# Kernel tuning notes

Hardware: AMD Instinct MI355X
Metric: run time of the kernel (lower is better)

The kernel has to match this reference:

```python
import jax, jax.numpy as jnp
import numpy as np

K_SIZE = 7   # kernel_size
DIL = 2      # dilation
PAD = 6      # padding; satisfies 2*PAD == DIL*(K_SIZE-1) so unfold L == H*W


def _unfold(x, k, d, p):
    # Mimics F.pad(mode='replicate') + nn.Unfold(kernel, dilation=d, stride=1)
    # followed by view(B, C, k*k, H, W). Channel-major, kernel rows then cols.
    B, C, H, W = x.shape
    xp = jnp.pad(x, ((0, 0), (0, 0), (p, p), (p, p)), mode='edge')
    cols = jnp.stack(
        [xp[:, :, i * d:i * d + H, j * d:j * d + W]
         for i in range(k) for j in range(k)], axis=2)
    return cols  # [B, C, k*k, H, W]


def setup_inputs() -> dict:
    key = jax.random.key(0)
    ks = jax.random.split(key, 5)
    B, Cin, Cout, H, W = 2, 64, 64, 128, 128
    x = jax.random.normal(ks[0], (B, Cin, H, W), jnp.float32)
    s_in = 1.0 / np.sqrt(Cin)
    s_out = 1.0 / np.sqrt(Cout)
    Wk = jax.random.uniform(ks[1], (Cout, Cin), jnp.float32, -s_in, s_in)
    Wq = jax.random.uniform(ks[2], (Cout, Cin), jnp.float32, -s_in, s_in)
    Wv = jax.random.uniform(ks[3], (Cout, Cin), jnp.float32, -s_in, s_in)
    Wt = jax.random.uniform(ks[4], (Cin, Cout), jnp.float32, -s_out, s_out)
    return {"x": x, "Wk": Wk, "Wq": Wq, "Wv": Wv, "Wt": Wt}


def reference(x, Wk, Wq, Wv, Wt):
    # 1x1 convs (bias=False) as channel contractions + ReLU
    K = jax.nn.relu(jnp.einsum('oi,bihw->bohw', Wk, x))
    Q = jax.nn.relu(jnp.einsum('oi,bihw->bohw', Wq, x))
    V = jax.nn.relu(jnp.einsum('oi,bihw->bohw', Wv, x))
    Ku = _unfold(K, K_SIZE, DIL, PAD)   # [B, C, k2, H, W]
    Vu = _unfold(V, K_SIZE, DIL, PAD)   # [B, C, k2, H, W]
    # scores over the k2 dilated neighbors of each pixel (q dim == 1)
    A = jnp.einsum('bckhw,bchw->bkhw', Ku, Q)
    A = jax.nn.softmax(A, axis=1)       # softmax over k2 (torch dim=1)
    out = jnp.einsum('bckhw,bkhw->bchw', Vu, A)
    return jnp.einsum('oi,bihw->bohw', Wt, out) + x
```

## Files before the change

### kernel.cpp

```cpp
#include <hip/hip_runtime.h>
#include <hip/hip_bf16.h>

#define HH 128
#define WW 128
#define HWSZ (HH * WW)
#define CC 64
#define BB 2
#define KK 7
#define K2 49
#define ROWE 280

typedef unsigned int u32;

__device__ __forceinline__ int clampi(int v, int lo, int hi) {
    return v < lo ? lo : (v > hi ? hi : v);
}

__device__ __forceinline__ uint4 ld16(const __hip_bfloat16* src) {
    uint4 d; __builtin_memcpy(&d, src, 16); return d;
}

__device__ __forceinline__ void unpack8(uint4 d, float* f) {
    f[0] = __uint_as_float(d.x << 16); f[1] = __uint_as_float(d.x & 0xffff0000u);
    f[2] = __uint_as_float(d.y << 16); f[3] = __uint_as_float(d.y & 0xffff0000u);
    f[4] = __uint_as_float(d.z << 16); f[5] = __uint_as_float(d.z & 0xffff0000u);
    f[6] = __uint_as_float(d.w << 16); f[7] = __uint_as_float(d.w & 0xffff0000u);
}

__device__ __forceinline__ unsigned short f2bf(float v) {
    __hip_bfloat16 b = __float2bfloat16(v);
    return *reinterpret_cast<unsigned short*>(&b);
}

__device__ __forceinline__ int lane_off(int w) {
    const int parity = w & 1, t = w >> 1, phase = t & 1;
    return parity * 140 + phase * 70 + (t - phase);
}

__global__ __launch_bounds__(256) void kqv_kernel(
    const float* __restrict__ x,  const float* __restrict__ Wk,
    const float* __restrict__ Wq, const float* __restrict__ Wv,
    __hip_bfloat16* __restrict__ Kp, __hip_bfloat16* __restrict__ Qt,
    __hip_bfloat16* __restrict__ Vp)
{
    __shared__ __align__(16) float Wl[64][32];
    __shared__ __hip_bfloat16 T[32][2][128];

    const int xcd   = blockIdx.x & 7;
    const int t     = blockIdx.x >> 3;
    const int pbl   = t & 15;
    const int slice = t >> 4;
    const int pb    = xcd * 16 + pbl;
    const int a     = slice >> 1;
    const int ohb   = (slice & 1) * 32;
    const int b0    = pb >> 6;
    const int h0    = 2 * (pb & 63);
    const int hw0   = (pb & 63) * 256;

    const float* Wsel = (a == 0) ? Wk : (a == 1) ? Wq : Wv;

    for (int idx = threadIdx.x; idx < 2048; idx += 256) {
        const int c  = idx >> 5;
        const int ol = idx & 31;
        Wl[c][ol] = Wsel[(ohb + ol) * CC + c];
    }
    __syncthreads();

    const int quad = threadIdx.x & 63;
    const int oct  = threadIdx.x >> 6;

    const float* xbase = x + (size_t)b0 * CC * HWSZ + hw0 + quad * 4;

    float acc[8][4];
#pragma unroll
    for (int i = 0; i < 8; ++i)
#pragma unroll
        for (int j = 0; j < 4; ++j) acc[i][j] = 0.f;

#pragma unroll 4
    for (int c = 0; c < CC; ++c) {
        const float4 x4 = *(const float4*)(xbase + (size_t)c * HWSZ);
        const float xj[4] = {x4.x, x4.y, x4.z, x4.w};
        float w8[8];
        *(float4*)(w8)     = *(const float4*)&Wl[c][oct * 8];
        *(float4*)(w8 + 4) = *(const float4*)&Wl[c][oct * 8 + 4];
#pragma unroll
        for (int i = 0; i < 8; ++i)
#pragma unroll
            for (int j = 0; j < 4; ++j)
                acc[i][j] = fmaf(w8[i], xj[j], acc[i][j]);
    }

#pragma unroll
    for (int i = 0; i < 8; ++i) {
        const int ol = oct * 8 + i;
#pragma unroll
        for (int j = 0; j < 4; ++j) {
            const int px = quad * 4 + j;
            T[ol][px >> 7][px & 127] = __float2bfloat16(fmaxf(acc[i][j], 0.f));
        }
    }
    __syncthreads();

    if (a == 1) {
        for (int idx = threadIdx.x; idx < 1024; idx += 256) {
            const int px = idx >> 2;
            const int ck = idx & 3;
            unsigned short e[8];
#pragma unroll
            for (int u = 0; u < 8; ++u) {
                __hip_bfloat16 bv = T[ck * 8 + u][px >> 7][px & 127];
                e[u] = *reinterpret_cast<unsigned short*>(&bv);
            }
            __hip_bfloat16* dst = Qt +
                (size_t)(b0 * HWSZ + hw0 + px) * CC + ohb + ck * 8;
            __builtin_memcpy(dst, e, 16);
        }
    } else {
        __hip_bfloat16* arrp = (a == 0) ? Kp : Vp;
        for (int idx = threadIdx.x; idx < 2240; idx += 256) {
            const int row_id = idx / 35;
            const int cki    = idx - row_id * 35;
            const int ol     = row_id >> 1;
            const int rr     = row_id & 1;
            unsigned short e[8];
#pragma unroll
            for (int u = 0; u < 8; ++u) {
                const int q      = cki * 8 + u;
                const int parity = q >= 140 ? 1 : 0;
                const int sslot  = q - parity * 140;
                const int phase  = sslot >= 70 ? 1 : 0;
                const int local  = sslot - phase * 70;
                const int pix    = clampi(2 * (local - (phase ? 2 : 3)) + parity,
                                          0, 127);
                __hip_bfloat16 bv = T[ol][rr][pix];
                e[u] = *reinterpret_cast<unsigned short*>(&bv);
            }
            __hip_bfloat16* dst = arrp +
                ((size_t)(b0 * CC + ohb + ol) * HH + (h0 + rr)) * ROWE + cki * 8;
            __builtin_memcpy(dst, e, 16);
        }
    }
}

__global__ __launch_bounds__(256) void attn_kernel(
    const __hip_bfloat16* __restrict__ Kp, const __hip_bfloat16* __restrict__ Qt,
    const __hip_bfloat16* __restrict__ Vp, const float* __restrict__ Wt,
    const float* __restrict__ x, float* __restrict__ out)
{
    __shared__ float part[2][K2][33];
    __shared__ __align__(16) float Wt_l[64][65];
    __shared__ __align__(16) __hip_bfloat16 O_l[32][72];

    const int xcd  = blockIdx.x & 7;
    const int s    = blockIdx.x >> 3;
    const int bh   = xcd * 32 + (s >> 2);
    const int wseg = s & 3;
    const int b    = bh >> 7;
    const int h    = bh & 127;

    const int tid = threadIdx.x;
    const int px  = (tid & 15) | ((tid >> 7) << 4);
    const int cq  = (tid >> 4) & 7;
    const int w   = wseg * 32 + px;
    const int p   = b * HWSZ + h * WW + w;
    const int c0  = cq * 8;

    for (int idx = tid; idx < 4096; idx += 256)
        Wt_l[idx >> 6][idx & 63] = Wt[idx];

    int hn[KK];
#pragma unroll
    for (int i = 0; i < KK; ++i) hn[i] = clampi(h + 2 * i - 6, 0, HH - 1);

    const int loff = lane_off(w);
    const size_t cstride = (size_t)HH * ROWE;
    const __hip_bfloat16* Kc = Kp + (size_t)(b * CC + c0) * cstride + loff;
    const __hip_bfloat16* Vc = Vp + (size_t)(b * CC + c0) * cstride + loff;

    float qf[8];
    unpack8(ld16(Qt + (size_t)p * CC + c0), qf);

    float sc[K2];
#pragma unroll
    for (int k = 0; k < K2; ++k) sc[k] = 0.f;

    for (int ci = 0; ci < 8; ++ci) {
        uint4 kd[KK];
        const __hip_bfloat16* base = Kc + (size_t)ci * cstride;
#pragma unroll
        for (int i = 0; i < KK; ++i) kd[i] = ld16(base + (size_t)hn[i] * ROWE);
        const float qv = qf[ci];
#pragma unroll
        for (int i = 0; i < KK; ++i) {
            float kf[8];
            unpack8(kd[i], kf);
#pragma unroll
            for (int j = 0; j < KK; ++j)
                sc[i * KK + j] = fmaf(kf[j], qv, sc[i * KK + j]);
        }
    }

#pragma unroll
    for (int k = 0; k < K2; ++k) sc[k] += __shfl_xor(sc[k], 16, 64);
#pragma unroll
    for (int k = 0; k < K2; ++k) sc[k] += __shfl_xor(sc[k], 32, 64);

    const int sl = (tid >> 6) & 1;
    if (((tid >> 4) & 3) == 0) {
#pragma unroll
        for (int k = 0; k < K2; ++k) part[sl][k][px] = sc[k];
    }
    __syncthreads();

#pragma unroll
    for (int k = 0; k < K2; ++k) sc[k] = part[0][k][px] + part[1][k][px];
    float m = sc[0];
#pragma unroll
    for (int k = 1; k < K2; ++k) m = fmaxf(m, sc[k]);
    float sum = 0.f;
#pragma unroll
    for (int k = 0; k < K2; ++k) { sc[k] = __expf(sc[k] - m); sum += sc[k]; }
    const float inv = 1.f / sum;
#pragma unroll
    for (int k = 0; k < K2; ++k) sc[k] *= inv;

    const int hw = h * WW + w;
    float fin[8];
#pragma unroll
    for (int i = 0; i < 8; ++i)
        fin[i] = x[((size_t)(b * CC) + c0 + i) * HWSZ + hw];

    unsigned short ob[8];
    for (int ci = 0; ci < 8; ++ci) {
        uint4 vd[KK];
        const __hip_bfloat16* base = Vc + (size_t)ci * cstride;
#pragma unroll
        for (int i = 0; i < KK; ++i) vd[i] = ld16(base + (size_t)hn[i] * ROWE);
        float acc = 0.f;
#pragma unroll
        for (int i = 0; i < KK; ++i) {
            float vf[8];
            unpack8(vd[i], vf);
#pragma unroll
            for (int j = 0; j < KK; ++j)
                acc = fmaf(vf[j], sc[i * KK + j], acc);
        }
        ob[ci] = f2bf(acc);
    }

    u32 od[4];
#pragma unroll
    for (int i = 0; i < 4; ++i)
        od[i] = (u32)ob[2 * i] | ((u32)ob[2 * i + 1] << 16);
    __builtin_memcpy(&O_l[px][c0], od, 16);
    __syncthreads();

#pragma unroll
    for (int c8 = 0; c8 < 8; ++c8) {
        uint4 d = *(const uint4*)&O_l[px][c8 * 8];
        float oc[8];
        unpack8(d, oc);
#pragma unroll
        for (int cc = 0; cc < 8; ++cc) {
            const int c = c8 * 8 + cc;
#pragma unroll
            for (int i = 0; i < 8; ++i)
                fin[i] = fmaf(Wt_l[c0 + i][c], oc[cc], fin[i]);
        }
    }

#pragma unroll
    for (int i = 0; i < 8; ++i)
        out[((size_t)(b * CC) + c0 + i) * HWSZ + hw] = fin[i];
}

extern "C" void kernel_launch(void* const* d_in, const int* in_sizes, int n_in,
                              void* d_out, int out_size, void* d_ws, size_t ws_size,
                              hipStream_t stream)
{
    const float* x  = (const float*)d_in[0];
    const float* Wk = (const float*)d_in[1];
    const float* Wq = (const float*)d_in[2];
    const float* Wv = (const float*)d_in[3];
    const float* Wt = (const float*)d_in[4];
    float* out = (float*)d_out;

    const size_t KP_ELEMS = (size_t)BB * CC * HH * ROWE;
    __hip_bfloat16* Kp = (__hip_bfloat16*)d_ws;
    __hip_bfloat16* Vp = Kp + KP_ELEMS;
    __hip_bfloat16* Qt = Vp + KP_ELEMS;

    hipLaunchKernelGGL(kqv_kernel, dim3(768), dim3(256), 0, stream,
                       x, Wk, Wq, Wv, Kp, Qt, Vp);
    hipLaunchKernelGGL(attn_kernel, dim3(1024), dim3(256), 0, stream,
                       Kp, Qt, Vp, Wt, x, out);
}
```

Baseline: 65.58 us.

## Fuse K/Q/V projections into one block per image row to reuse x loads

```diff
diff --git a/kernel.cpp b/kernel.cpp
--- a/kernel.cpp
+++ b/kernel.cpp
@@ -37,108 +37,107 @@
     return parity * 140 + phase * 70 + (t - phase);
 }
 
-__global__ __launch_bounds__(256) void kqv_kernel(
+__global__ __launch_bounds__(1024) void kqv_kernel(
     const float* __restrict__ x,  const float* __restrict__ Wk,
     const float* __restrict__ Wq, const float* __restrict__ Wv,
     __hip_bfloat16* __restrict__ Kp, __hip_bfloat16* __restrict__ Qt,
     __hip_bfloat16* __restrict__ Vp)
 {
-    __shared__ __align__(16) float Wl[64][32];
-    __shared__ __hip_bfloat16 T[32][2][128];
-
-    const int xcd   = blockIdx.x & 7;
-    const int t     = blockIdx.x >> 3;
-    const int pbl   = t & 15;
-    const int slice = t >> 4;
-    const int pb    = xcd * 16 + pbl;
-    const int a     = slice >> 1;
-    const int ohb   = (slice & 1) * 32;
-    const int b0    = pb >> 6;
-    const int h0    = 2 * (pb & 63);
-    const int hw0   = (pb & 63) * 256;
-
-    const float* Wsel = (a == 0) ? Wk : (a == 1) ? Wq : Wv;
-
-    for (int idx = threadIdx.x; idx < 2048; idx += 256) {
-        const int c  = idx >> 5;
-        const int ol = idx & 31;
-        Wl[c][ol] = Wsel[(ohb + ol) * CC + c];
+    __shared__ __align__(16) float Wl[64][192];
+    __shared__ __hip_bfloat16 T[64][128];
+
+    const int xcd = blockIdx.x & 7;
+    const int s   = blockIdx.x >> 3;
+    const int rid = xcd * 32 + s;
+    const int b   = rid >> 7;
+    const int h   = rid & 127;
+
+    const int tid  = threadIdx.x;
+    const int duo  = tid & 63;
+    const int oset = tid >> 6;
+    const int oc0  = oset * 4;
+
+    for (int idx = tid; idx < 64 * 192; idx += 1024) {
+        const int c   = idx / 192;
+        const int col = idx - c * 192;
+        const int a   = col >> 6;
+        const int och = col & 63;
+        const float* Wa = (a == 0) ? Wk : (a == 1) ? Wq : Wv;
+        Wl[c][col] = Wa[och * CC + c];
     }
     __syncthreads();
 
-    const int quad = threadIdx.x & 63;
-    const int oct  = threadIdx.x >> 6;
-
-    const float* xbase = x + (size_t)b0 * CC * HWSZ + hw0 + quad * 4;
-
-    float acc[8][4];
-#pragma unroll
-    for (int i = 0; i < 8; ++i)
-#pragma unroll
-        for (int j = 0; j < 4; ++j) acc[i][j] = 0.f;
+    const float* xrow = x + (size_t)b * CC * HWSZ + h * WW + duo * 2;
+
+    float acc[3][4][2];
+#pragma unroll
+    for (int a = 0; a < 3; ++a)
+#pragma unroll
+        for (int i = 0; i < 4; ++i)
+#pragma unroll
+            for (int j = 0; j < 2; ++j) acc[a][i][j] = 0.f;
 
 #pragma unroll 4
     for (int c = 0; c < CC; ++c) {
-        const float4 x4 = *(const float4*)(xbase + (size_t)c * HWSZ);
-        const float xj[4] = {x4.x, x4.y, x4.z, x4.w};
-        float w8[8];
-        *(float4*)(w8)     = *(const float4*)&Wl[c][oct * 8];
-        *(float4*)(w8 + 4) = *(const float4*)&Wl[c][oct * 8 + 4];
-#pragma unroll
-        for (int i = 0; i < 8; ++i)
-#pragma unroll
-            for (int j = 0; j < 4; ++j)
-                acc[i][j] = fmaf(w8[i], xj[j], acc[i][j]);
-    }
-
-#pragma unroll
-    for (int i = 0; i < 8; ++i) {
-        const int ol = oct * 8 + i;
-#pragma unroll
-        for (int j = 0; j < 4; ++j) {
-            const int px = quad * 4 + j;
-            T[ol][px >> 7][px & 127] = __float2bfloat16(fmaxf(acc[i][j], 0.f));
-        }
-    }
-    __syncthreads();
-
-    if (a == 1) {
-        for (int idx = threadIdx.x; idx < 1024; idx += 256) {
-            const int px = idx >> 2;
-            const int ck = idx & 3;
+        const float2 x2 = *(const float2*)(xrow + (size_t)c * HWSZ);
+        const float xj[2] = {x2.x, x2.y};
+#pragma unroll
+        for (int a = 0; a < 3; ++a) {
+            const float4 w4 = *(const float4*)&Wl[c][a * 64 + oc0];
+            const float wi[4] = {w4.x, w4.y, w4.z, w4.w};
+#pragma unroll
+            for (int i = 0; i < 4; ++i)
+#pragma unroll
+                for (int j = 0; j < 2; ++j)
+                    acc[a][i][j] = fmaf(wi[i], xj[j], acc[a][i][j]);
+        }
+    }
+
+#pragma unroll
+    for (int a = 0; a < 3; ++a) {
+        __syncthreads();
+#pragma unroll
+        for (int i = 0; i < 4; ++i)
+#pragma unroll
+            for (int j = 0; j < 2; ++j)
+                T[oc0 + i][duo * 2 + j] =
+                    __float2bfloat16(fmaxf(acc[a][i][j], 0.f));
+        __syncthreads();
+
+        if (a == 1) {
+            const int px = tid >> 3;
+            const int ck = tid & 7;
             unsigned short e[8];
 #pragma unroll
             for (int u = 0; u < 8; ++u) {
-                __hip_bfloat16 bv = T[ck * 8 + u][px >> 7][px & 127];
+                __hip_bfloat16 bv = T[ck * 8 + u][px];
                 e[u] = *reinterpret_cast<unsigned short*>(&bv);
             }
             __hip_bfloat16* dst = Qt +
-                (size_t)(b0 * HWSZ + hw0 + px) * CC + ohb + ck * 8;
+                (size_t)(b * HWSZ + h * WW + px) * CC + ck * 8;
             __builtin_memcpy(dst, e, 16);
-        }
-    } else {
-        __hip_bfloat16* arrp = (a == 0) ? Kp : Vp;
-        for (int idx = threadIdx.x; idx < 2240; idx += 256) {
-            const int row_id = idx / 35;
-            const int cki    = idx - row_id * 35;
-            const int ol     = row_id >> 1;
-            const int rr     = row_id & 1;
-            unsigned short e[8];
-#pragma unroll
-            for (int u = 0; u < 8; ++u) {
-                const int q      = cki * 8 + u;
-                const int parity = q >= 140 ? 1 : 0;
-                const int sslot  = q - parity * 140;
-                const int phase  = sslot >= 70 ? 1 : 0;
-                const int local  = sslot - phase * 70;
-                const int pix    = clampi(2 * (local - (phase ? 2 : 3)) + parity,
-                                          0, 127);
-                __hip_bfloat16 bv = T[ol][rr][pix];
-                e[u] = *reinterpret_cast<unsigned short*>(&bv);
+        } else {
+            __hip_bfloat16* arrp = (a == 0) ? Kp : Vp;
+            for (int idx = tid; idx < 64 * 35; idx += 1024) {
+                const int och = idx / 35;
+                const int cki = idx - och * 35;
+                unsigned short e[8];
+#pragma unroll
+                for (int u = 0; u < 8; ++u) {
+                    const int q      = cki * 8 + u;
+                    const int parity = q >= 140 ? 1 : 0;
+                    const int sslot  = q - parity * 140;
+                    const int phase  = sslot >= 70 ? 1 : 0;
+                    const int local  = sslot - phase * 70;
+                    const int pix    = clampi(
+                        2 * (local - (phase ? 2 : 3)) + parity, 0, 127);
+                    __hip_bfloat16 bv = T[och][pix];
+                    e[u] = *reinterpret_cast<unsigned short*>(&bv);
+                }
+                __hip_bfloat16* dst = arrp +
+                    ((size_t)(b * CC + och) * HH + h) * ROWE + cki * 8;
+                __builtin_memcpy(dst, e, 16);
             }
-            __hip_bfloat16* dst = arrp +
-                ((size_t)(b0 * CC + ohb + ol) * HH + (h0 + rr)) * ROWE + cki * 8;
-            __builtin_memcpy(dst, e, 16);
         }
     }
 }
@@ -291,7 +290,7 @@
     __hip_bfloat16* Vp = Kp + KP_ELEMS;
     __hip_bfloat16* Qt = Vp + KP_ELEMS;
 
-    hipLaunchKernelGGL(kqv_kernel, dim3(768), dim3(256), 0, stream,
+    hipLaunchKernelGGL(kqv_kernel, dim3(256), dim3(1024), 0, stream,
                        x, Wk, Wq, Wv, Kp, Qt, Vp);
     hipLaunchKernelGGL(attn_kernel, dim3(1024), dim3(256), 0, stream,
                        Kp, Qt, Vp, Wt, x, out);
```

After: 70.14 us. +6.9%, slower.
